# Kernel tuning notes

Hardware: AMD Instinct MI355X
Metric: run time of the kernel (lower is better)

Reference implementation:

```python
import jax, jax.numpy as jnp
import numpy as np

N, E, G, H, IN, OUT, L = 50000, 800000, 512, 128, 128, 10, 3
TH = 0.01  # filter_perm threshold


def setup_inputs() -> dict:
    key = jax.random.key(0)
    ks = jax.random.split(key, 16)
    s = 0.05
    return {
        "x": jax.random.normal(ks[0], (N, IN), jnp.float32),
        "edge_index": jax.random.randint(ks[1], (2, E), 0, N, jnp.int32),
        "batch": jnp.sort(jax.random.randint(ks[2], (N,), 0, G, jnp.int32)),
        "lin1_W": jax.random.normal(ks[3], (IN, H), jnp.float32) * s,
        "lin1_b": jnp.zeros((H,), jnp.float32),
        # per layer: [gcn_W, sage_Wn, sage_Ws, gin_W, gconv_Ws, gconv_Wn]
        "gnn_W": jax.random.normal(ks[4], (L, 6, H, H), jnp.float32) * s,
        "pool_p": jax.random.normal(ks[5], (L, 2, H), jnp.float32) * s,
        "lin_out_W": jax.random.normal(ks[6], (H, H), jnp.float32) * s,
        "lin_out_b": jnp.zeros((H,), jnp.float32),
        "cls_W": jax.random.normal(ks[7], (H, OUT), jnp.float32) * s,
        "cls_b": jnp.zeros((OUT,), jnp.float32),
        "na_log": 0.001 * jax.random.normal(ks[8], (L, 4), jnp.float32),
        "pool_log": 0.001 * jax.random.normal(ks[9], (L, 3), jnp.float32),
        "readout_log": 0.001 * jax.random.normal(ks[10], (L + 1, 3), jnp.float32),
        "la_log": 0.001 * jax.random.normal(ks[11], (1, 3), jnp.float32),
    }


def _readout(h, batch, w):
    # mixed readout: w0*mean + w1*max + w2*sum over graphs
    ssum = jax.ops.segment_sum(h, batch, num_segments=G)
    cnt = jax.ops.segment_sum(jnp.ones((h.shape[0], 1), h.dtype), batch, num_segments=G)
    mean = ssum / jnp.maximum(cnt, 1.0)
    smax = jax.ops.segment_max(h, batch, num_segments=G)
    smax = jnp.where(jnp.isfinite(smax), smax, 0.0)
    return w[0] * mean + w[1] * smax + w[2] * ssum


def reference(x, edge_index, batch, lin1_W, lin1_b, gnn_W, pool_p,
              lin_out_W, lin_out_b, cls_W, cls_b,
              na_log, pool_log, readout_log, la_log):
    na_a = jax.nn.softmax(na_log, -1)
    pool_a = jax.nn.softmax(pool_log, -1)
    ro_a = jax.nn.softmax(readout_log, -1)
    la_a = jax.nn.softmax(la_log, -1)

    # add self loops
    ar = jnp.arange(N, dtype=edge_index.dtype)
    src = jnp.concatenate([edge_index[0], ar])
    dst = jnp.concatenate([edge_index[1], ar])
    ew = jnp.ones(src.shape[0], jnp.float32)

    h = jax.nn.elu(x @ lin1_W + lin1_b)
    reps = [_readout(h, batch, ro_a[0])]

    for i in range(L):
        W = gnn_W[i]
        deg = jnp.maximum(jax.ops.segment_sum(ew, dst, num_segments=N), 1e-6)
        s_agg = jax.ops.segment_sum(h[src] * ew[:, None], dst, num_segments=N)  # [N,H]
        # gcn: symmetric-normalized aggregation of transformed features
        hg = h @ W[0]
        norm = ew * jax.lax.rsqrt(deg)[src] * jax.lax.rsqrt(deg)[dst]
        gcn = jax.ops.segment_sum(hg[src] * norm[:, None], dst, num_segments=N)
        sage = (s_agg / deg[:, None]) @ W[1] + h @ W[2]
        gin = (h + s_agg) @ W[3]
        gconv = h @ W[4] + s_agg @ W[5]
        a = na_a[i]
        h = a[0] * gcn + a[1] * sage + a[2] * gin + a[3] * gconv
        h = jax.nn.elu(h)
        # LayerNorm over the FULL tensor (normalized_shape = x.size()), no affine
        m = h.mean()
        v = jnp.mean((h - m) ** 2)
        h = (h - m) * jax.lax.rsqrt(v + 1e-5)
        # dropout identity (eval mode)
        # mixed pooling: score-gated soft pooling + filter_perm threshold mask
        g1 = jax.nn.sigmoid(h @ pool_p[i, 0])
        g2 = jnp.tanh(h @ pool_p[i, 1])
        pa = pool_a[i]
        gate = pa[0] * g1 + pa[1] * g2 + pa[2]  # third op = 'none' (gate 1)
        keep = (gate > TH).astype(h.dtype)
        h = h * (gate * keep)[:, None]
        ew = ew * keep[src] * keep[dst]
        reps.append(_readout(h, batch, ro_a[i + 1]))

    R = jnp.stack(reps)  # [L+1, G, H]
    la = la_a[0]
    z = la[0] * jax.nn.elu(R.sum(0)) + la[1] * jax.nn.elu(R.mean(0)) + la[2] * jax.nn.elu(R.max(0))
    z = jax.nn.elu(z @ lin_out_W + lin_out_b)
    logits = z @ cls_W + cls_b
    return jax.nn.log_softmax(logits, -1)
```

## Files before the change

### kernel.cpp

```cpp
#include <hip/hip_runtime.h>
#include <math.h>

#define NN 50000
#define EE 800000
#define GG 512
#define HH 128
#define LL 3
#define OUTC 10
#define THR 0.01f

typedef unsigned short u16;
typedef unsigned int u32;
typedef __attribute__((ext_vector_type(8))) short short8;
typedef __attribute__((ext_vector_type(4))) float f32x4;

__device__ __forceinline__ float elu_f(float x){ return x > 0.f ? x : (expf(x)-1.f); }
__device__ __forceinline__ u16 f2bf(float f){
    u32 u = __float_as_uint(f);
    return (u16)((u + 0x7fffu + ((u>>16)&1u)) >> 16);
}
__device__ __forceinline__ float bf2f(u16 b){ return __uint_as_float(((u32)b)<<16); }
__device__ __forceinline__ u32 pack2(float a, float b){
    return (u32)f2bf(a) | ((u32)f2bf(b)<<16);
}


__device__ void softmax_row(const float* in, float* out, int c){
    float m = in[0];
    for (int j=1;j<c;++j) m = fmaxf(m, in[j]);
    float s = 0.f;
    for (int j=0;j<c;++j){ float e = expf(in[j]-m); out[j]=e; s+=e; }
    for (int j=0;j<c;++j) out[j] /= s;
}

__global__ void prep_coef_k(const float* __restrict__ na, const float* __restrict__ pl,
                            const float* __restrict__ ro, const float* __restrict__ la,
                            float* __restrict__ coef){
    if (threadIdx.x != 0 || blockIdx.x != 0) return;
    for (int i=0;i<LL;++i)   softmax_row(na + i*4, coef + i*4, 4);
    for (int i=0;i<LL;++i)   softmax_row(pl + i*3, coef + 12 + i*3, 3);
    for (int i=0;i<LL+1;++i) softmax_row(ro + i*3, coef + 21 + i*3, 3);
    softmax_row(la, coef + 33, 3);
}

__global__ __launch_bounds__(256) void prep_w_k(const float* __restrict__ gW,
                                                const float* __restrict__ lin1W,
                                                const float* __restrict__ coef,
                                                u16* __restrict__ Wc, u16* __restrict__ lin1t){
    int idx = blockIdx.x*256 + threadIdx.x;
    const int total = LL*4*16384;
    if (idx < total){
        int i = idx >> 16;
        int rem = idx & 65535;
        int p = rem >> 14;
        int j = rem & 16383;
        int n = j >> 7, k = j & 127;
        const float* W = gW + (size_t)i*6*16384;
        float a0=coef[i*4], a1=coef[i*4+1], a2=coef[i*4+2], a3=coef[i*4+3];
        int e = k*128 + n;
        float v;
        if (p==0)      v = a1*W[2*16384+e] + a2*W[3*16384+e] + a3*W[4*16384+e];
        else if (p==1) v = a2*W[3*16384+e] + a3*W[5*16384+e];
        else if (p==2) v = a1*W[1*16384+e];
        else           v = a0*W[0*16384+e];
        Wc[(size_t)(i*4+p)*16384 + n*128 + k] = f2bf(v);
    } else if (idx < total + 16384){
        int j = idx - total;
        int n = j >> 7, k = j & 127;
        lin1t[n*128 + k] = f2bf(lin1W[k*128 + n]);
    }
}

__global__ void x2bf_k(const float* __restrict__ x, u16* __restrict__ xb){
    int i = blockIdx.x*256 + threadIdx.x;
    if (i >= NN*HH/8) return;
    const float4* p = (const float4*)x + (size_t)i*2;
    float4 v0 = p[0], v1 = p[1];
    uint4 o;
    o.x = pack2(v0.x, v0.y); o.y = pack2(v0.z, v0.w);
    o.z = pack2(v1.x, v1.y); o.w = pack2(v1.z, v1.w);
    ((uint4*)xb)[i] = o;
}

__global__ void count_k(const int* __restrict__ dst, int* __restrict__ counts){
    int e = blockIdx.x*256 + threadIdx.x;
    if (e < EE) atomicAdd(&counts[dst[e]], 1);
}

__global__ __launch_bounds__(256) void scan1_k(const int* __restrict__ counts,
                                               int* __restrict__ pre, int* __restrict__ bsum){
    int b = blockIdx.x, t = threadIdx.x;
    int base = b*1024 + t*4;
    int4 v = make_int4(0,0,0,0);
    if (base + 3 < NN) v = *(const int4*)(counts + base);
    else {
        int* pv = (int*)&v;
        #pragma unroll
        for (int j=0;j<4;++j) pv[j] = (base+j < NN) ? counts[base+j] : 0;
    }
    v.x = (v.x+3)&~3; v.y = (v.y+3)&~3; v.z = (v.z+3)&~3; v.w = (v.w+3)&~3;
    int s0 = v.x, s1 = s0+v.y, s2 = s1+v.z, s3 = s2+v.w;
    int lane = t & 63, w = t >> 6;
    int incl = s3;
    #pragma unroll
    for (int o=1;o<64;o<<=1){
        int u = __shfl_up(incl, o, 64);
        if (lane >= o) incl += u;
    }
    __shared__ int wsum[4];
    if (lane == 63) wsum[w] = incl;
    __syncthreads();
    int woff = 0;
    #pragma unroll
    for (int i=0;i<4;++i) if (i < w) woff += wsum[i];
    int excl = woff + incl - s3;
    int4 o4 = make_int4(excl, excl+s0, excl+s1, excl+s2);
    if (base + 3 < NN) *(int4*)(pre + base) = o4;
    else {
        int* po = (int*)&o4;
        for (int j=0;j<4;++j) if (base+j < NN) pre[base+j] = po[j];
    }
    if (t == 255) bsum[b] = woff + incl;
}

__global__ __launch_bounds__(256) void scan3_k(const int* __restrict__ pre,
                                               const int* __restrict__ bsum,
                                               int* __restrict__ row_ptr, int* __restrict__ cursor){
    int b = blockIdx.x, t = threadIdx.x;
    __shared__ int boff_s;
    if (t < 64){
        int v = (t < b) ? bsum[t] : 0;
        #pragma unroll
        for (int o=32;o>0;o>>=1) v += __shfl_down(v, o, 64);
        if (t == 0) boff_s = v;
    }
    __syncthreads();
    int boff = boff_s;
    int base = b*1024;
    #pragma unroll
    for (int j=0;j<4;++j){
        int i = base + j*256 + t;
        if (i < NN){
            int r = pre[i] + boff;
            row_ptr[i] = r;
            cursor[i] = r;
        }
    }
    if (b == (int)gridDim.x - 1 && t == 0) row_ptr[NN] = boff + bsum[b];
}

__global__ void init_alive_k(float* __restrict__ a){
    int i = blockIdx.x*256 + threadIdx.x;
    if (i <= NN) a[i] = (i < NN) ? 1.f : 0.f;
}

__global__ void fill_k(const int* __restrict__ src, const int* __restrict__ dst,
                       int* __restrict__ cursor, int* __restrict__ csr_src){
    int e = blockIdx.x*256 + threadIdx.x;
    if (e < EE){
        int p = atomicAdd(&cursor[dst[e]], 1);
        csr_src[p] = src[e];
    }
}

__global__ void pad_fill_k(const int* __restrict__ cursor, const int* __restrict__ row_ptr,
                           int* __restrict__ csr_src){
    int n = blockIdx.x*256 + threadIdx.x;
    if (n >= NN) return;
    int e1 = row_ptr[n+1];
    for (int p = cursor[n]; p < e1; ++p) csr_src[p] = NN;
}

__global__ void gstart_k(const int* __restrict__ batch, int* __restrict__ gstart){
    int g = blockIdx.x*256 + threadIdx.x;
    if (g > GG) return;
    if (g == GG){ gstart[GG] = NN; return; }
    int lo = 0, hi = NN;
    while (lo < hi){
        int mid = (lo + hi) >> 1;
        if (batch[mid] < g) lo = mid + 1; else hi = mid;
    }
    gstart[g] = lo;
}

template<int FLAGS, int NP>
__global__ __launch_bounds__(256) void mm_k(
    const u16* __restrict__ A0, const u16* __restrict__ A1,
    const u16* __restrict__ A2, const u16* __restrict__ A3,
    const u16* __restrict__ Bb, const float* __restrict__ rowscale,
    const float* __restrict__ bias,
    u16* __restrict__ Cbf, double* __restrict__ stats, int M)
{
    int tid = threadIdx.x;
    int w = tid >> 6, l = tid & 63;
    int row0 = blockIdx.x * 128;
    int rbase = row0 + w*32 + (l & 15);
    int kq = l >> 4;
    const short8 zz = {0,0,0,0,0,0,0,0};

    f32x4 acc[2][8];
    #pragma unroll
    for (int rt=0;rt<2;++rt)
        #pragma unroll
        for (int ct=0;ct<8;++ct) acc[rt][ct] = (f32x4){0.f,0.f,0.f,0.f};

    auto do_pair = [&](const u16* __restrict__ Ap, const u16* __restrict__ Bp){
        #pragma unroll
        for (int ks=0; ks<4; ++ks){
            int ko = (ks*4 + kq)*8;
            short8 a[2], b[8];
            #pragma unroll
            for (int rt=0; rt<2; ++rt){
                int gr = rbase + rt*16;
                a[rt] = (gr < M) ? *(const short8*)(Ap + (size_t)gr*128 + ko) : zz;
            }
            #pragma unroll
            for (int ct=0; ct<8; ++ct)
                b[ct] = *(const short8*)(Bp + (ct*16 + (l&15))*128 + ko);
            #pragma unroll
            for (int rt=0; rt<2; ++rt)
                #pragma unroll
                for (int ct=0; ct<8; ++ct)
                    acc[rt][ct] = __builtin_amdgcn_mfma_f32_16x16x32_bf16(a[rt], b[ct], acc[rt][ct], 0, 0, 0);
        }
    };

    if constexpr (NP == 4){
        do_pair(A2, Bb + 2*16384);
        #pragma unroll
        for (int rt=0; rt<2; ++rt){
            #pragma unroll
            for (int i=0; i<4; ++i){
                int row = row0 + w*32 + rt*16 + (l>>4)*4 + i;
                float d = (row < M) ? rowscale[row] : 0.f;
                #pragma unroll
                for (int ct=0; ct<8; ++ct) acc[rt][ct][i] *= d;
            }
        }
        do_pair(A0, Bb);
        do_pair(A1, Bb + 16384);
        do_pair(A3, Bb + 3*16384);
    } else {
        do_pair(A0, Bb);
    }

    float ls = 0.f, lq = 0.f;
    float bcol[8];
    if constexpr (FLAGS & 2){
        #pragma unroll
        for (int ct=0; ct<8; ++ct) bcol[ct] = bias[ct*16 + (l&15)];
    }
    #pragma unroll
    for (int rt=0; rt<2; ++rt){
        #pragma unroll
        for (int i=0; i<4; ++i){
            int row = row0 + w*32 + rt*16 + (l>>4)*4 + i;
            if (row >= M) continue;
            #pragma unroll
            for (int ct=0; ct<8; ++ct){
                float v = acc[rt][ct][i];
                if constexpr (FLAGS & 2) v += bcol[ct];
                v = elu_f(v);
                Cbf[(size_t)row*128 + ct*16 + (l&15)] = f2bf(v);
                if constexpr (FLAGS & 1){ ls += v; lq = fmaf(v, v, lq); }
            }
        }
    }
    if constexpr (FLAGS & 1){
        double s = ls, q = lq;
        #pragma unroll
        for (int o=32;o>0;o>>=1){ s += __shfl_xor(s,o,64); q += __shfl_xor(q,o,64); }
        __shared__ double sw[4], qw[4];
        if (l == 0){ sw[w] = s; qw[w] = q; }
        __syncthreads();
        if (tid == 0){
            atomicAdd(&stats[0], sw[0]+sw[1]+sw[2]+sw[3]);
            atomicAdd(&stats[1], qw[0]+qw[1]+qw[2]+qw[3]);
        }
    }
}


__global__ __launch_bounds__(256) void deg2_k(const int* __restrict__ rp, const int* __restrict__ cs,
                                              const float* __restrict__ alive,
                                              float2* __restrict__ ar2, float* __restrict__ invdeg){
    if (blockIdx.x == 0 && threadIdx.x == 0) ar2[NN] = make_float2(0.f, 0.f);
    int n = (blockIdx.x*256 + threadIdx.x) >> 6;
    int lane = threadIdx.x & 63;
    if (n >= NN) return;
    int e0 = rp[n], e1 = rp[n+1];
    float c = 0.f;
    for (int e = e0 + lane; e < e1; e += 64) c += alive[cs[e]];
    #pragma unroll
    for (int o=32;o>0;o>>=1) c += __shfl_xor(c, o, 64);
    if (lane == 0){
        float al = alive[n];
        float d = (al == 0.f) ? 1e-6f : fmaxf(1.f + c, 1e-6f);
        ar2[n] = make_float2(al, al * rsqrtf(d));
        invdeg[n] = 1.f / d;
    }
}

__global__ __launch_bounds__(64) void agg_k(const u16* __restrict__ h,
    const int* __restrict__ rp, const int* __restrict__ cs,
    const float2* __restrict__ ar2,
    u16* __restrict__ sagg, u16* __restrict__ gagg){
    int n = blockIdx.x;
    int lane = threadIdx.x;
    float2 an = ar2[n];
    u32* so = (u32*)(sagg + (size_t)n*HH);
    u32* go = (u32*)(gagg + (size_t)n*HH);
    if (an.x == 0.f){ so[lane]=0u; go[lane]=0u; return; }
    float rn = an.y;
    int e0 = rp[n], e1 = rp[n+1];
    float sx=0.f, sy=0.f, gx=0.f, gy=0.f;
    for (int e = e0; e < e1; e += 4){
        int i0 = cs[e], i1 = cs[e+1], i2 = cs[e+2], i3 = cs[e+3];
        float2 w0 = ar2[i0], w1 = ar2[i1], w2 = ar2[i2], w3 = ar2[i3];
        u32 h0 = *(const u32*)(h + (size_t)i0*HH + lane*2);
        u32 h1 = *(const u32*)(h + (size_t)i1*HH + lane*2);
        u32 h2 = *(const u32*)(h + (size_t)i2*HH + lane*2);
        u32 h3 = *(const u32*)(h + (size_t)i3*HH + lane*2);
        float ax, ay;
        ax = bf2f((u16)(h0 & 0xffffu)); ay = bf2f((u16)(h0 >> 16));
        sx = fmaf(w0.x, ax, sx); sy = fmaf(w0.x, ay, sy);
        gx = fmaf(w0.y, ax, gx); gy = fmaf(w0.y, ay, gy);
        ax = bf2f((u16)(h1 & 0xffffu)); ay = bf2f((u16)(h1 >> 16));
        sx = fmaf(w1.x, ax, sx); sy = fmaf(w1.x, ay, sy);
        gx = fmaf(w1.y, ax, gx); gy = fmaf(w1.y, ay, gy);
        ax = bf2f((u16)(h2 & 0xffffu)); ay = bf2f((u16)(h2 >> 16));
        sx = fmaf(w2.x, ax, sx); sy = fmaf(w2.x, ay, sy);
        gx = fmaf(w2.y, ax, gx); gy = fmaf(w2.y, ay, gy);
        ax = bf2f((u16)(h3 & 0xffffu)); ay = bf2f((u16)(h3 >> 16));
        sx = fmaf(w3.x, ax, sx); sy = fmaf(w3.x, ay, sy);
        gx = fmaf(w3.y, ax, gx); gy = fmaf(w3.y, ay, gy);
    }
    u32 hn = *(const u32*)(h + (size_t)n*HH + lane*2);
    float hx = bf2f((u16)(hn & 0xffffu)), hy = bf2f((u16)(hn >> 16));
    sx += hx; sy += hy;
    gx = fmaf(rn, hx, gx); gy = fmaf(rn, hy, gy);
    so[lane] = pack2(sx, sy);
    go[lane] = pack2(rn*gx, rn*gy);
}

__global__ __launch_bounds__(1024) void lnro_k(u16* __restrict__ hb,
                                               const double* __restrict__ stats,
                                               const float* __restrict__ p0,
                                               const float* __restrict__ p1,
                                               const float* __restrict__ pa,
                                               const float* __restrict__ row,
                                               const int* __restrict__ gstart,
                                               float* __restrict__ alive,
                                               float* __restrict__ rep){
    int g = blockIdx.x, tid = threadIdx.x;
    int w = tid >> 6, lane = tid & 63;
    int beg = gstart[g], end = gstart[g+1];
    const double tot = (double)NN * (double)HH;
    double m = stats[0] / tot;
    double var = stats[1] / tot - m*m;
    float mf = (float)m;
    float rs = rsqrtf((float)var + 1e-5f);
    float2 q0 = ((const float2*)p0)[lane];
    float2 q1 = ((const float2*)p1)[lane];
    float pa0 = pa[0], pa1 = pa[1], pa2 = pa[2];
    float csx = 0.f, csy = 0.f, cmx = -INFINITY, cmy = -INFINITY;
    for (int n = beg + w; n < end; n += 16){
        u32 hv = ((u32*)(hb + (size_t)n*HH))[lane];
        float vx = (bf2f((u16)(hv & 0xffffu)) - mf) * rs;
        float vy = (bf2f((u16)(hv >> 16))    - mf) * rs;
        float d0 = vx*q0.x + vy*q0.y;
        float d1 = vx*q1.x + vy*q1.y;
        #pragma unroll
        for (int o=32;o>0;o>>=1){ d0 += __shfl_xor(d0,o,64); d1 += __shfl_xor(d1,o,64); }
        float g1 = 1.f/(1.f + expf(-d0));
        float g2 = tanhf(d1);
        float gate = pa0*g1 + pa1*g2 + pa2;
        float keep = gate > THR ? 1.f : 0.f;
        float sc = gate*keep;
        vx *= sc; vy *= sc;
        ((u32*)(hb + (size_t)n*HH))[lane] = pack2(vx, vy);
        if (lane == 0 && keep == 0.f) alive[n] = 0.f;
        csx += vx; csy += vy;
        cmx = fmaxf(cmx, vx); cmy = fmaxf(cmy, vy);
    }
    __shared__ float ls[16][HH];
    __shared__ float lm[16][HH];
    ls[w][2*lane] = csx; ls[w][2*lane+1] = csy;
    lm[w][2*lane] = cmx; lm[w][2*lane+1] = cmy;
    __syncthreads();
    if (tid < HH){
        float s = 0.f, mx = -INFINITY;
        #pragma unroll
        for (int i=0;i<16;++i){ s += ls[i][tid]; mx = fmaxf(mx, lm[i][tid]); }
        if (mx == -INFINITY) mx = 0.f;
        float cnt = (float)(end - beg);
        float mean = s / fmaxf(cnt, 1.f);
        rep[(size_t)g*HH + tid] = row[0]*mean + row[1]*mx + row[2]*s;
    }
}

__global__ __launch_bounds__(1024) void readout_k(const u16* __restrict__ h,
                                                  const int* __restrict__ gstart,
                                                  const float* __restrict__ w,
                                                  float* __restrict__ rep){
    int g = blockIdx.x;
    int t = threadIdx.x & 127, q = threadIdx.x >> 7;
    int beg = gstart[g], end = gstart[g+1];
    float sum = 0.f, mx = -INFINITY;
    for (int n = beg + q; n < end; n += 8){
        float v = bf2f(h[(size_t)n*HH + t]);
        sum += v;
        mx = fmaxf(mx, v);
    }
    __shared__ float ss[8][HH];
    __shared__ float ms[8][HH];
    ss[q][t] = sum; ms[q][t] = mx;
    __syncthreads();
    if (threadIdx.x < HH){
        float s = 0.f, m = -INFINITY;
        #pragma unroll
        for (int i=0;i<8;++i){ s += ss[i][threadIdx.x]; m = fmaxf(m, ms[i][threadIdx.x]); }
        if (m == -INFINITY) m = 0.f;
        float cnt = (float)(end - beg);
        float mean = s / fmaxf(cnt, 1.f);
        rep[(size_t)g*HH + threadIdx.x] = w[0]*mean + w[1]*m + w[2]*s;
    }
}

__global__ __launch_bounds__(128) void final_k(const float* __restrict__ reps,
                                               const float* __restrict__ la,
                                               const float* __restrict__ loW,
                                               const float* __restrict__ lob,
                                               const float* __restrict__ cW,
                                               const float* __restrict__ cb,
                                               float* __restrict__ out){
    int g = blockIdx.x, t = threadIdx.x;
    float r0 = reps[(size_t)(0*GG+g)*HH + t];
    float r1 = reps[(size_t)(1*GG+g)*HH + t];
    float r2 = reps[(size_t)(2*GG+g)*HH + t];
    float r3 = reps[(size_t)(3*GG+g)*HH + t];
    float s = r0+r1+r2+r3;
    float mean = 0.25f*s;
    float mx = fmaxf(fmaxf(r0,r1), fmaxf(r2,r3));
    float z = la[0]*elu_f(s) + la[1]*elu_f(mean) + la[2]*elu_f(mx);
    __shared__ float zs[HH];
    zs[t] = z;
    __syncthreads();
    float a = lob[t];
    for (int k=0;k<HH;++k) a = fmaf(zs[k], loW[(size_t)k*HH + t], a);
    float z2 = elu_f(a);
    __shared__ float z2s[HH];
    z2s[t] = z2;
    __syncthreads();
    __shared__ float lg[OUTC];
    if (t < OUTC){
        float acc = cb[t];
        for (int k=0;k<HH;++k) acc = fmaf(z2s[k], cW[(size_t)k*OUTC + t], acc);
        lg[t] = acc;
    }
    __syncthreads();
    if (t == 0){
        float m = lg[0];
        for (int o=1;o<OUTC;++o) m = fmaxf(m, lg[o]);
        float se = 0.f;
        for (int o=0;o<OUTC;++o) se += expf(lg[o]-m);
        float lse = m + logf(se);
        for (int o=0;o<OUTC;++o) out[(size_t)g*OUTC + o] = lg[o] - lse;
    }
}


extern "C" void kernel_launch(void* const* d_in, const int* in_sizes, int n_in,
                              void* d_out, int out_size, void* d_ws, size_t ws_size,
                              hipStream_t stream){
    const float* x     = (const float*)d_in[0];
    const int*   ei    = (const int*)d_in[1];
    const int*   batch = (const int*)d_in[2];
    const float* l1W   = (const float*)d_in[3];
    const float* l1b   = (const float*)d_in[4];
    const float* gW    = (const float*)d_in[5];
    const float* poolp = (const float*)d_in[6];
    const float* loW   = (const float*)d_in[7];
    const float* lob   = (const float*)d_in[8];
    const float* cW    = (const float*)d_in[9];
    const float* cb    = (const float*)d_in[10];
    const float* nalog = (const float*)d_in[11];
    const float* pllog = (const float*)d_in[12];
    const float* rolog = (const float*)d_in[13];
    const float* lalog = (const float*)d_in[14];
    float* out = (float*)d_out;

    char* wsb = (char*)d_ws;
    size_t off = 0;
    auto alloc = [&](size_t bytes)->char* {
        char* p = wsb + off;
        off += (bytes + 255) & ~(size_t)255;
        return p;
    };
    const int EEP = EE + 3*NN + 16;
    u16*   hb     = (u16*)alloc(sizeof(u16)*(size_t)(NN+1)*HH);
    u16*   xb     = (u16*)alloc(sizeof(u16)*(size_t)NN*HH);
    u16*   sagg   = (u16*)alloc(sizeof(u16)*(size_t)NN*HH);
    u16*   gagg   = (u16*)alloc(sizeof(u16)*(size_t)NN*HH);
    u16*   Wc     = (u16*)alloc(sizeof(u16)*(size_t)LL*4*HH*HH);
    u16*   lin1t  = (u16*)alloc(sizeof(u16)*HH*HH);
    int*   row_ptr= (int*)alloc(sizeof(int)*(NN+1));
    int*   counts = (int*)alloc(sizeof(int)*NN);
    int*   cursor = (int*)alloc(sizeof(int)*NN);
    int*   pre    = (int*)alloc(sizeof(int)*NN);
    int*   bsum   = (int*)alloc(sizeof(int)*64);
    int*   csr_src= (int*)alloc(sizeof(int)*EEP);
    float2* ar2   = (float2*)alloc(sizeof(float2)*(NN+1));
    float* invdeg = (float*)alloc(sizeof(float)*NN);
    float* alive  = (float*)alloc(sizeof(float)*(NN+1));
    int*   gstart = (int*)alloc(sizeof(int)*(GG+1));
    float* reps   = (float*)alloc(sizeof(float)*(size_t)(LL+1)*GG*HH);
    float* coef   = (float*)alloc(sizeof(float)*64);
    double* stats = (double*)alloc(sizeof(double)*2*LL);

    const int* srcp = ei;
    const int* dstp = ei + EE;

    hipMemsetAsync(counts, 0, sizeof(int)*NN, stream);
    hipMemsetAsync(stats, 0, sizeof(double)*2*LL, stream);

    const int SCAN_BLOCKS = (NN + 1023)/1024;

    prep_coef_k<<<1, 64, 0, stream>>>(nalog, pllog, rolog, lalog, coef);
    prep_w_k<<<(LL*4*16384 + 16384 + 255)/256, 256, 0, stream>>>(gW, l1W, coef, Wc, lin1t);
    count_k<<<(EE + 255)/256, 256, 0, stream>>>(dstp, counts);
    scan1_k<<<SCAN_BLOCKS, 256, 0, stream>>>(counts, pre, bsum);
    scan3_k<<<SCAN_BLOCKS, 256, 0, stream>>>(pre, bsum, row_ptr, cursor);
    fill_k<<<(EE + 255)/256, 256, 0, stream>>>(srcp, dstp, cursor, csr_src);
    pad_fill_k<<<(NN + 255)/256, 256, 0, stream>>>(cursor, row_ptr, csr_src);
    gstart_k<<<(GG + 256)/256, 256, 0, stream>>>(batch, gstart);
    init_alive_k<<<(NN + 256)/256, 256, 0, stream>>>(alive);
    x2bf_k<<<(NN*HH/8 + 255)/256, 256, 0, stream>>>(x, xb);

    const int gemm_blocks = (NN + 127)/128;

    mm_k<2,1><<<gemm_blocks, 256, 0, stream>>>(xb, nullptr, nullptr, nullptr,
                                               lin1t, nullptr, l1b, hb, nullptr, NN);
    readout_k<<<GG, 1024, 0, stream>>>(hb, gstart, coef + 21, reps);

    for (int i=0;i<LL;++i){
        deg2_k<<<(NN + 3)/4, 256, 0, stream>>>(row_ptr, csr_src, alive, ar2, invdeg);
        agg_k<<<NN, 64, 0, stream>>>(hb, row_ptr, csr_src, ar2, sagg, gagg);
        mm_k<1,4><<<gemm_blocks, 256, 0, stream>>>(hb, sagg, sagg, gagg,
                                                   Wc + (size_t)i*4*16384, invdeg, nullptr,
                                                   hb, stats + 2*i, NN);
        lnro_k<<<GG, 1024, 0, stream>>>(hb, stats + 2*i,
                                        poolp + (size_t)(i*2+0)*HH,
                                        poolp + (size_t)(i*2+1)*HH,
                                        coef + 12 + i*3,
                                        coef + 21 + (i+1)*3,
                                        gstart, alive,
                                        reps + (size_t)(i+1)*GG*HH);
    }

    final_k<<<GG, HH, 0, stream>>>(reps, coef + 33, loW, lob, cW, cb, out);
}
```

Measured before the change: 566.1 us.

## Stage GEMM weight tiles in swizzled shared memory with double buffering

```diff
diff --git a/kernel.cpp b/kernel.cpp
--- a/kernel.cpp
+++ b/kernel.cpp
@@ -191,6 +191,7 @@
     const float* __restrict__ bias,
     u16* __restrict__ Cbf, double* __restrict__ stats, int M)
 {
+    __shared__ u16 Bs[2][128*128];
     int tid = threadIdx.x;
     int w = tid >> 6, l = tid & 63;
     int row0 = blockIdx.x * 128;
@@ -204,19 +205,36 @@
         #pragma unroll
         for (int ct=0;ct<8;++ct) acc[rt][ct] = (f32x4){0.f,0.f,0.f,0.f};
 
-    auto do_pair = [&](const u16* __restrict__ Ap, const u16* __restrict__ Bp){
+    uint4 st[8];
+    auto stage_load = [&](const u16* __restrict__ Bp){
+        #pragma unroll
+        for (int i=0;i<8;++i)
+            st[i] = *(const uint4*)(Bp + (i*256 + tid)*8);
+    };
+    auto stage_write = [&](int buf){
+        #pragma unroll
+        for (int i=0;i<8;++i){
+            int c = i*256 + tid;
+            int n = c >> 4, kc = c & 15;
+            *(uint4*)((char*)&Bs[buf][0] + n*256 + ((kc ^ (n&7))<<4)) = st[i];
+        }
+    };
+
+    auto compute = [&](int buf, const u16* __restrict__ Ap){
         #pragma unroll
         for (int ks=0; ks<4; ++ks){
-            int ko = (ks*4 + kq)*8;
+            int kc = ks*4 + kq;
             short8 a[2], b[8];
             #pragma unroll
             for (int rt=0; rt<2; ++rt){
                 int gr = rbase + rt*16;
-                a[rt] = (gr < M) ? *(const short8*)(Ap + (size_t)gr*128 + ko) : zz;
+                a[rt] = (gr < M) ? *(const short8*)(Ap + (size_t)gr*128 + kc*8) : zz;
             }
             #pragma unroll
-            for (int ct=0; ct<8; ++ct)
-                b[ct] = *(const short8*)(Bp + (ct*16 + (l&15))*128 + ko);
+            for (int ct=0; ct<8; ++ct){
+                int nf = ct*16 + (l&15);
+                b[ct] = *(const short8*)((const char*)&Bs[buf][0] + nf*256 + ((kc ^ (nf&7))<<4));
+            }
             #pragma unroll
             for (int rt=0; rt<2; ++rt)
                 #pragma unroll
@@ -226,7 +244,10 @@
     };
 
     if constexpr (NP == 4){
-        do_pair(A2, Bb + 2*16384);
+        stage_load(Bb + 2*16384); stage_write(0);
+        __syncthreads();
+        stage_load(Bb);
+        compute(0, A2);
         #pragma unroll
         for (int rt=0; rt<2; ++rt){
             #pragma unroll
@@ -237,11 +258,21 @@
                 for (int ct=0; ct<8; ++ct) acc[rt][ct][i] *= d;
             }
         }
-        do_pair(A0, Bb);
-        do_pair(A1, Bb + 16384);
-        do_pair(A3, Bb + 3*16384);
+        stage_write(1);
+        __syncthreads();
+        stage_load(Bb + 16384);
+        compute(1, A0);
+        stage_write(0);
+        __syncthreads();
+        stage_load(Bb + 3*16384);
+        compute(0, A1);
+        stage_write(1);
+        __syncthreads();
+        compute(1, A3);
     } else {
-        do_pair(A0, Bb);
+        stage_load(Bb); stage_write(0);
+        __syncthreads();
+        compute(0, A0);
     }
 
     float ls = 0.f, lq = 0.f;
```

Result: faster. 514.0 us (-9.2%).
